# Optimization experiments

Hardware: AMD Instinct MI355X
Metric: run time of the kernel (lower is better)

Reference implementation:

```python
import jax, jax.numpy as jnp
import numpy as np

B, D, CIN, H, W = 2, 6, 3, 96, 96
DIM, NUM_HEADS, DEPTH = 144, 6, 2
WS = (2, 8, 8)   # window size (d, h, w)
SS = (1, 4, 4)   # shift size for odd blocks
HID = int(DIM * 2.0)
TBL = (2 * WS[0] - 1) * (2 * WS[1] - 1) * (2 * WS[2] - 1)  # 675
EPS = 1e-5


def _rpi(ws):
    # pairwise relative position index, same math as WindowAttention.get_position_index
    coords = np.stack(np.meshgrid(np.arange(ws[0]), np.arange(ws[1]), np.arange(ws[2]), indexing='ij'))
    cf = coords.reshape(3, -1).astype(np.int64)
    rc = (cf[:, :, None] - cf[:, None, :]).transpose(1, 2, 0)
    rc[..., 0] += ws[0] - 1
    rc[..., 1] += ws[1] - 1
    rc[..., 2] += ws[2] - 1
    rc[..., 0] *= (2 * ws[1] - 1) * (2 * ws[2] - 1)
    rc[..., 1] *= 2 * ws[2] - 1
    return rc.sum(-1)  # (N, N)


def _win_part_np(x, ws):
    b, d, h, w, c = x.shape
    x = x.reshape(b, d // ws[0], ws[0], h // ws[1], ws[1], w // ws[2], ws[2], c)
    return x.transpose(0, 1, 3, 5, 2, 4, 6, 7).reshape(-1, ws[0] * ws[1] * ws[2], c)


def _attn_mask(Dp, Hp, Wp, ws, ss):
    # static shift-window attention mask, same as compute_mask
    img = np.zeros((1, Dp, Hp, Wp, 1), np.float32)
    cnt = 0
    for d in (slice(-ws[0]), slice(-ws[0], -ss[0]), slice(-ss[0], None)):
        for h in (slice(-ws[1]), slice(-ws[1], -ss[1]), slice(-ss[1], None)):
            for w in (slice(-ws[2]), slice(-ws[2], -ss[2]), slice(-ss[2], None)):
                img[:, d, h, w, :] = cnt
                cnt += 1
    mw = _win_part_np(img, ws)[..., 0]  # (nW, N)
    am = mw[:, None, :] - mw[:, :, None]
    return np.where(am != 0, np.float32(-100.0), np.float32(0.0))


RPI = jnp.asarray(_rpi(WS))            # (N, N) int
MASK = jnp.asarray(_attn_mask(D, H, W, WS, SS))  # (nW, N, N)


def _ln(x, g, b):
    mu = jnp.mean(x, -1, keepdims=True)
    var = jnp.mean(jnp.square(x - mu), -1, keepdims=True)
    return (x - mu) * jax.lax.rsqrt(var + EPS) * g + b


def _win_part(x, ws):
    b, d, h, w, c = x.shape
    x = x.reshape(b, d // ws[0], ws[0], h // ws[1], ws[1], w // ws[2], ws[2], c)
    return x.transpose(0, 1, 3, 5, 2, 4, 6, 7).reshape(-1, ws[0] * ws[1] * ws[2], c)


def _win_rev(xw, ws, b, d, h, w):
    x = xw.reshape(b, d // ws[0], h // ws[1], w // ws[2], ws[0], ws[1], ws[2], -1)
    return x.transpose(0, 1, 4, 2, 5, 3, 6, 7).reshape(b, d, h, w, -1)


def _stl(x, i, shifted, params):
    # one Swin Transformer Layer; x: (B, D, H, W, C)
    n1g, n1b, qkvw, qkvb, rpb, projw, projb, n2g, n2b, fc1w, fc1b, fc2w, fc2b = params
    b, d, h, w, c = x.shape
    hd = c // NUM_HEADS
    scale = hd ** -0.5
    y = _ln(x, n1g[i], n1b[i])
    if shifted:
        y = jnp.roll(y, (-SS[0], -SS[1], -SS[2]), axis=(1, 2, 3))
    xw = _win_part(y, WS)  # (B_, N, C)
    B_, N, _ = xw.shape
    qkv = jnp.einsum('bnc,oc->bno', xw, qkvw[i]) + qkvb[i]
    qkv = qkv.reshape(B_, N, 3, NUM_HEADS, hd).transpose(2, 0, 3, 1, 4)
    q, k, v = qkv[0], qkv[1], qkv[2]
    attn = jnp.einsum('bhnd,bhmd->bhnm', q * scale, k)
    bias = rpb[i][RPI].transpose(2, 0, 1)  # (heads, N, N)
    attn = attn + bias[None]
    if shifted:
        nW = MASK.shape[0]
        attn = attn.reshape(B_ // nW, nW, NUM_HEADS, N, N) + MASK[None, :, None]
        attn = attn.reshape(B_, NUM_HEADS, N, N)
    attn = jax.nn.softmax(attn, axis=-1)
    out = jnp.einsum('bhnm,bhmd->bhnd', attn, v).transpose(0, 2, 1, 3).reshape(B_, N, c)
    out = jnp.einsum('bnc,oc->bno', out, projw[i]) + projb[i]
    y = _win_rev(out, WS, b, d, h, w)
    if shifted:
        y = jnp.roll(y, (SS[0], SS[1], SS[2]), axis=(1, 2, 3))
    x = x + y
    z = _ln(x, n2g[i], n2b[i])
    z = jnp.einsum('bdhwc,oc->bdhwo', z, fc1w[i]) + fc1b[i]
    z = jax.nn.gelu(z, approximate=False)
    z = jnp.einsum('bdhwo,co->bdhwc', z, fc2w[i]) + fc2b[i]
    return x + z


def setup_inputs() -> dict:
    key = jax.random.key(0)
    ks = jax.random.split(key, 8)
    s = 0.02
    return {
        'x': jax.random.normal(ks[0], (B, D, CIN, H, W), jnp.float32),
        'conv_w': jax.random.normal(ks[1], (DIM, CIN, 1, 3, 3), jnp.float32) * s,
        'conv_b': jnp.zeros((DIM,), jnp.float32),
        'ln0_g': jnp.ones((DIM,), jnp.float32),
        'ln0_b': jnp.zeros((DIM,), jnp.float32),
        'n1g': jnp.ones((DEPTH, DIM), jnp.float32),
        'n1b': jnp.zeros((DEPTH, DIM), jnp.float32),
        'qkvw': jax.random.normal(ks[2], (DEPTH, 3 * DIM, DIM), jnp.float32) * s,
        'qkvb': jnp.zeros((DEPTH, 3 * DIM), jnp.float32),
        'rpb': jax.random.normal(ks[3], (DEPTH, TBL, NUM_HEADS), jnp.float32) * s,
        'projw': jax.random.normal(ks[4], (DEPTH, DIM, DIM), jnp.float32) * s,
        'projb': jnp.zeros((DEPTH, DIM), jnp.float32),
        'n2g': jnp.ones((DEPTH, DIM), jnp.float32),
        'n2b': jnp.zeros((DEPTH, DIM), jnp.float32),
        'fc1w': jax.random.normal(ks[5], (DEPTH, HID, DIM), jnp.float32) * s,
        'fc1b': jnp.zeros((DEPTH, HID), jnp.float32),
        'fc2w': jax.random.normal(ks[6], (DEPTH, DIM, HID), jnp.float32) * s,
        'fc2b': jnp.zeros((DEPTH, DIM), jnp.float32),
        'lin_w': jax.random.normal(ks[7], (DIM, DIM), jnp.float32) * s,
        'lin_b': jnp.zeros((DIM,), jnp.float32),
        'ln1_g': jnp.ones((DIM,), jnp.float32),
        'ln1_b': jnp.zeros((DIM,), jnp.float32),
    }


def reference(x, conv_w, conv_b, ln0_g, ln0_b, n1g, n1b, qkvw, qkvb, rpb, projw, projb,
              n2g, n2b, fc1w, fc1b, fc2w, fc2b, lin_w, lin_b, ln1_g, ln1_b):
    # x: (n, d, c, h, w)
    y = x.transpose(0, 2, 1, 3, 4)  # n c d h w
    y = jax.lax.conv_general_dilated(
        y, conv_w, (1, 1, 1), [(0, 0), (1, 1), (1, 1)],
        dimension_numbers=('NCDHW', 'OIDHW', 'NCDHW')) + conv_b[None, :, None, None, None]
    y = y.transpose(0, 2, 3, 4, 1)  # n d h w c
    y = _ln(y, ln0_g, ln0_b)
    y = y.transpose(0, 4, 1, 2, 3)  # n c d h w
    params = (n1g, n1b, qkvw, qkvb, rpb, projw, projb, n2g, n2b, fc1w, fc1b, fc2w, fc2b)
    # RSTB (num_blocks = 1): residual group (STG of DEPTH STLs) + linear + skip
    f = y.transpose(0, 2, 3, 4, 1)  # b d h w c
    for i in range(DEPTH):
        f = _stl(f, i, i % 2 == 1, params)
    f = jnp.einsum('bdhwc,oc->bdhwo', f, lin_w) + lin_b
    y = y + f.transpose(0, 4, 1, 2, 3)
    # trailing LayerNorm and rearrange back to (n, d, c, h, w)
    out = _ln(y.transpose(0, 2, 3, 4, 1), ln1_g, ln1_b)
    return out.transpose(0, 1, 4, 2, 3)
```

## Files before the change

### kernel.cpp

```cpp
#include <hip/hip_runtime.h>
#include <math.h>

#define NTOK 110592
#define NWIN 864
#define TS   15925248

typedef unsigned short u16;
typedef unsigned int   u32;
typedef __attribute__((ext_vector_type(8))) short short8;
typedef __attribute__((ext_vector_type(4))) float float4v;

__device__ __forceinline__ float bf2f(u16 v) { return __uint_as_float(((u32)v) << 16); }
__device__ __forceinline__ u16 f2bf(float f) {
    u32 u = __float_as_uint(f);
    u32 r = u + 0x7fffu + ((u >> 16) & 1u);
    return (u16)(r >> 16);
}
__device__ __forceinline__ void unpack2(u32 u, float& lo, float& hi) {
    lo = __uint_as_float(u << 16);
    hi = __uint_as_float(u & 0xffff0000u);
}
__device__ __forceinline__ u32 pack2(float lo, float hi) {
    return (u32)f2bf(lo) | ((u32)f2bf(hi) << 16);
}
__device__ __forceinline__ float wave_sum(float v) {
    #pragma unroll
    for (int o = 32; o > 0; o >>= 1) v += __shfl_xor(v, o, 64);
    return v;
}

__device__ __forceinline__ void win_to_src(int tw, int shifted, int& sb, int& sd, int& sh, int& sw) {
    int n = tw & 127;
    int win = tw >> 7;
    int ww = win % 12;
    int wh = (win / 12) % 12;
    int rest = win / 144;
    int wd = rest % 3;
    sb = rest / 3;
    int ld = n >> 6, lh = (n >> 3) & 7, lw = n & 7;
    int dr = wd * 2 + ld, hr = wh * 8 + lh, wr = ww * 8 + lw;
    if (shifted) {
        sd = (dr + 1) % 6;
        sh = (hr + 4) % 96;
        sw = (wr + 4) % 96;
    } else {
        sd = dr; sh = hr; sw = wr;
    }
}

__device__ __forceinline__ int tok_region(int t, int wdn, int whn, int wwn) {
    int dr = wdn * 2 + (t >> 6), hr = whn * 8 + ((t >> 3) & 7), wr = wwn * 8 + (t & 7);
    int rd = (dr < 4) ? 0 : ((dr < 5) ? 1 : 2);
    int rh = (hr < 88) ? 0 : ((hr < 92) ? 1 : 2);
    int rw = (wr < 88) ? 0 : ((wr < 92) ? 1 : 2);
    return rd * 9 + rh * 3 + rw;
}

__global__ __launch_bounds__(256) void convert_weights(
    const float* __restrict__ qkvw, const float* __restrict__ projw,
    const float* __restrict__ fc1w, const float* __restrict__ fc2w,
    const float* __restrict__ linw, u16* __restrict__ wbuf,
    const float* __restrict__ rpb, float* __restrict__ bexp)
{
    int i = blockIdx.x * 256 + threadIdx.x;
    if (i < 124416) wbuf[i] = f2bf(qkvw[i]);
    else if (i < 165888) wbuf[i] = f2bf(projw[i - 124416]);
    else if (i < 248832) wbuf[i] = f2bf(fc1w[i - 165888]);
    else if (i < 331776) wbuf[i] = f2bf(fc2w[i - 248832]);
    else if (i < 352512) wbuf[i] = f2bf(linw[i - 331776]);
    else if (i < 549120) {
        int k = i - 352512;
        int n = k & 127, m = (k >> 7) & 127;
        int lh = k >> 14;
        int h = lh % 6, l = lh / 6;
        int rdi = (m >> 6) - (n >> 6) + 1;
        int rhi = ((m >> 3) & 7) - ((n >> 3) & 7) + 7;
        int rwi = (m & 7) - (n & 7) + 7;
        int bi = (rdi * 15 + rhi) * 15 + rwi;
        bexp[k] = rpb[l * 4050 + bi * 6 + h];
    }
}

__global__ __launch_bounds__(256) void conv_ln0_row(
    const float* __restrict__ x, const float* __restrict__ cw, const float* __restrict__ cb,
    const float* __restrict__ g0, const float* __restrict__ b0,
    float* __restrict__ y0)
{
    int bh = blockIdx.x;
    int h = bh % 96, bd = bh / 96;
    int b = bd / 6, d = bd - b * 6;
    __shared__ float ws[192][29];
    __shared__ float xsr[9][100];
    __shared__ float cbias[192], gg[144], bbv[144];
    int tid = threadIdx.x;

    for (int i = tid; i < 9 * 98; i += 256) {
        int row = i / 98, wx = i - row * 98;
        int ci = row / 3, kh = row - 3 * ci;
        int hh = h + kh - 1, wsrc = wx - 1;
        float v = 0.f;
        if (hh >= 0 && hh < 96 && wsrc >= 0 && wsrc < 96)
            v = x[((((size_t)b * 6 + d) * 3 + ci) * 96 + hh) * 96 + wsrc];
        xsr[row][wx] = v;
    }
    for (int i = tid; i < 192 * 27; i += 256) {
        int c = i / 27, j = i - c * 27;
        ws[c][j] = (c < 144) ? cw[c * 27 + j] : 0.f;
    }
    for (int i = tid; i < 192; i += 256) cbias[i] = (i < 144) ? cb[i] : 0.f;
    for (int i = tid; i < 144; i += 256) { gg[i] = g0[i]; bbv[i] = b0[i]; }
    __syncthreads();

    int wv = tid >> 6, lane = tid & 63;
    int p0 = wv * 24;

    float a0[24], a1[24], a2[24];
    #pragma unroll
    for (int k = 0; k < 24; k++) {
        a0[k] = cbias[lane]; a1[k] = cbias[lane + 64]; a2[k] = cbias[lane + 128];
    }

    for (int cikh = 0; cikh < 9; cikh++) {
        const float* xr = &xsr[cikh][p0];
        float xv[26];
        #pragma unroll
        for (int t = 0; t < 26; t++) xv[t] = xr[t];
        #pragma unroll
        for (int kw = 0; kw < 3; kw++) {
            int j = cikh * 3 + kw;
            float w0 = ws[lane][j], w1 = ws[lane + 64][j], w2 = ws[lane + 128][j];
            #pragma unroll
            for (int k = 0; k < 24; k++) {
                float xvv = xv[k + kw];
                a0[k] += w0 * xvv; a1[k] += w1 * xvv; a2[k] += w2 * xvv;
            }
        }
    }

    #pragma unroll
    for (int k = 0; k < 24; k++) {
        int p = p0 + k;
        float v0 = a0[k], v1 = a1[k];
        float v2m = (lane < 16) ? a2[k] : 0.f;
        float s  = wave_sum(v0 + v1 + v2m);
        float s2 = wave_sum(v0 * v0 + v1 * v1 + v2m * v2m);
        float mu = s * (1.f / 144.f);
        float rstd = rsqrtf(fmaxf(s2 * (1.f / 144.f) - mu * mu, 0.f) + 1e-5f);
        size_t o = ((size_t)bh * 96 + p) * 144;
        float r0 = (v0 - mu) * rstd * gg[lane] + bbv[lane];
        float r1 = (v1 - mu) * rstd * gg[lane + 64] + bbv[lane + 64];
        y0[o + lane] = r0;
        y0[o + lane + 64] = r1;
        if (lane < 16) {
            float r2 = (a2[k] - mu) * rstd * gg[lane + 128] + bbv[lane + 128];
            y0[o + lane + 128] = r2;
        }
    }
}

template<int MODE>
__global__ __launch_bounds__(256) void ln_gather(
    const float* __restrict__ in, u16* __restrict__ out,
    const float* __restrict__ g, const float* __restrict__ bt)
{
    int tok = blockIdx.x * 4 + (threadIdx.x >> 6);
    int lane = threadIdx.x & 63;
    int src;
    {
        int b, d, h, w;
        win_to_src(tok, MODE == 2, b, d, h, w);
        src = ((b * 6 + d) * 96 + h) * 96 + w;
    }
    const float2* row = (const float2*)(in + (size_t)src * 144);
    float2 a = row[lane];
    float2 b2 = (lane < 8) ? row[64 + lane] : make_float2(0.f, 0.f);
    float s  = wave_sum(a.x + a.y + b2.x + b2.y);
    float s2 = wave_sum(a.x * a.x + a.y * a.y + b2.x * b2.x + b2.y * b2.y);
    float mu = s * (1.f / 144.f);
    float rstd = rsqrtf(fmaxf(s2 * (1.f / 144.f) - mu * mu, 0.f) + 1e-5f);
    const float2* g2 = (const float2*)g;
    const float2* t2 = (const float2*)bt;
    u32* orow = (u32*)(out + (size_t)tok * 144);
    float2 gg = g2[lane], tt = t2[lane];
    orow[lane] = pack2((a.x - mu) * rstd * gg.x + tt.x, (a.y - mu) * rstd * gg.y + tt.y);
    if (lane < 8) {
        float2 gh = g2[64 + lane], th = t2[64 + lane];
        orow[64 + lane] = pack2((b2.x - mu) * rstd * gh.x + th.x, (b2.y - mu) * rstd * gh.y + th.y);
    }
}

template<int AMODE, int EPI, int SHIFTED, int ADDBIAS, int KTILES>
__global__ __launch_bounds__(192) void mgemm(
    const void* __restrict__ Asrc, const u16* __restrict__ Wt, const float* __restrict__ bias,
    u16* __restrict__ outb, float* __restrict__ fres, const float* __restrict__ y0,
    const float* __restrict__ lng, const float* __restrict__ lnb,
    int a_add, int a_ld, int w_ld, int o_ld, int o_add)
{
    __shared__ u16 As[64 * 152];
    int m0 = blockIdx.y * 64, n0 = blockIdx.x * 144;
    int tid = threadIdx.x;
    int wv3 = tid / 64, lane = tid & 63;
    int mrow = lane & 15, quad = lane >> 4;
    const short8 z8 = {0, 0, 0, 0, 0, 0, 0, 0};

    float4v acc[4][3];
    #pragma unroll
    for (int i = 0; i < 4; i++)
        #pragma unroll
        for (int j = 0; j < 3; j++) acc[i][j] = (float4v){0.f, 0.f, 0.f, 0.f};

    #pragma unroll
    for (int kt = 0; kt < KTILES; kt++) {
        if (kt) __syncthreads();
        if constexpr (AMODE == 5) {
            __shared__ float gs[144], bs[144], ps[64][6];
            for (int i = tid; i < 144; i += 192) { gs[i] = lng[i]; bs[i] = lnb[i]; }
            int r = tid / 3, p = tid - 3 * r;
            int srow = a_add + m0 + r;
            const float4* s4 = (const float4*)((const float*)Asrc + (size_t)srow * 144) + p * 12;
            float4 av[12];
            float s = 0.f, s2 = 0.f;
            #pragma unroll
            for (int q = 0; q < 12; q++) {
                av[q] = s4[q];
                s  += (av[q].x + av[q].y) + (av[q].z + av[q].w);
                s2 += (av[q].x * av[q].x + av[q].y * av[q].y)
                    + (av[q].z * av[q].z + av[q].w * av[q].w);
            }
            ps[r][p] = s; ps[r][3 + p] = s2;
            __syncthreads();
            float S  = ps[r][0] + ps[r][1] + ps[r][2];
            float S2 = ps[r][3] + ps[r][4] + ps[r][5];
            float mu = S * (1.f / 144.f);
            float rstd = rsqrtf(fmaxf(S2 * (1.f / 144.f) - mu * mu, 0.f) + 1e-5f);
            #pragma unroll
            for (int q = 0; q < 12; q++) {
                int n = p * 48 + q * 4;
                *(u32*)&As[r * 152 + n]     = pack2((av[q].x - mu) * rstd * gs[n]     + bs[n],
                                                    (av[q].y - mu) * rstd * gs[n + 1] + bs[n + 1]);
                *(u32*)&As[r * 152 + n + 2] = pack2((av[q].z - mu) * rstd * gs[n + 2] + bs[n + 2],
                                                    (av[q].w - mu) * rstd * gs[n + 3] + bs[n + 3]);
            }
        } else if constexpr (AMODE == 2) {
            const u16* A = (const u16*)Asrc;
            #pragma unroll
            for (int idx = tid; idx < 1152; idx += 192) {
                int r = idx / 18, c4 = idx - r * 18;
                *(short8*)&As[r * 152 + c4 * 8] =
                    *(const short8*)&A[(size_t)(a_add + m0 + r) * a_ld + kt * 144 + c4 * 8];
            }
        } else if constexpr (AMODE == 3) {
            const u16* A = (const u16*)Asrc;
            int chtok = a_ld;
            int cc = m0 / chtok;
            int t0 = m0 - cc * chtok;
            const u16* Ac = A + (size_t)cc * chtok * 144;
            #pragma unroll
            for (int idx = tid; idx < 1152; idx += 192) {
                int r = idx / 18, c4 = idx - r * 18;
                int hh = c4 / 3, sub = c4 - hh * 3;
                *(short8*)&As[r * 152 + c4 * 8] =
                    *(const short8*)&Ac[((size_t)hh * chtok + t0 + r) * 24 + sub * 8];
            }
        } else {
            const float* A = (const float*)Asrc;
            #pragma unroll
            for (int idx = tid; idx < 2304; idx += 192) {
                int r = idx / 36, c4 = idx - r * 36;
                const float4* src4 = (const float4*)&A[(size_t)(a_add + m0 + r) * a_ld + kt * 144];
                float4 v = src4[c4];
                *(u32*)&As[r * 152 + c4 * 4]     = pack2(v.x, v.y);
                *(u32*)&As[r * 152 + c4 * 4 + 2] = pack2(v.z, v.w);
            }
        }
        __syncthreads();

        const u16* Wg = Wt + (size_t)(n0 + wv3 * 48 + mrow) * w_ld + kt * 144;

        #pragma unroll
        for (int ks = 0; ks < 4; ks++) {
            int k0 = ks * 32;
            short8 af[4], bf[3];
            #pragma unroll
            for (int i = 0; i < 4; i++)
                af[i] = *(const short8*)&As[(i * 16 + mrow) * 152 + k0 + quad * 8];
            #pragma unroll
            for (int j = 0; j < 3; j++)
                bf[j] = *(const short8*)&Wg[(size_t)j * 16 * w_ld + k0 + quad * 8];
            #pragma unroll
            for (int i = 0; i < 4; i++)
                #pragma unroll
                for (int j = 0; j < 3; j++)
                    acc[i][j] = __builtin_amdgcn_mfma_f32_16x16x32_bf16(af[i], bf[j], acc[i][j], 0, 0, 0);
        }
        {
            bool tl = (quad < 2);
            short8 af[4], bf[3];
            #pragma unroll
            for (int i = 0; i < 4; i++)
                af[i] = tl ? *(const short8*)&As[(i * 16 + mrow) * 152 + 128 + quad * 8] : z8;
            #pragma unroll
            for (int j = 0; j < 3; j++)
                bf[j] = tl ? *(const short8*)&Wg[(size_t)j * 16 * w_ld + 128 + quad * 8] : z8;
            #pragma unroll
            for (int i = 0; i < 4; i++)
                #pragma unroll
                for (int j = 0; j < 3; j++)
                    acc[i][j] = __builtin_amdgcn_mfma_f32_16x16x32_bf16(af[i], bf[j], acc[i][j], 0, 0, 0);
        }
    }

    if constexpr (EPI == 6) {
        __syncthreads();
        int slot = blockIdx.x;
        #pragma unroll
        for (int i = 0; i < 4; i++)
            #pragma unroll
            for (int reg = 0; reg < 4; reg++) {
                int ml = i * 16 + quad * 4 + reg;
                #pragma unroll
                for (int j = 0; j < 3; j++) {
                    int hn = wv3 * 48 + j * 16 + mrow;
                    float v = acc[i][j][reg];
                    if (ADDBIAS) v += bias[n0 + hn];
                    if (slot == 0) v *= 0.20412414523193154f;
                    As[ml * 152 + hn] = f2bf(v);
                }
            }
        __syncthreads();
        int chtok = o_ld;
        u32* outw = (u32*)outb;
        for (int gi = tid; gi < 4608; gi += 192) {
            int hh = gi / 768;
            int rem = gi - hh * 768;
            int t = rem / 12, dd2 = rem - t * 12;
            outw[(size_t)slot * 72 * chtok + ((size_t)hh * chtok + m0 + t) * 12 + dd2]
                = *(const u32*)&As[t * 152 + hh * 24 + dd2 * 2];
        }
    } else {
        #pragma unroll
        for (int i = 0; i < 4; i++) {
            #pragma unroll
            for (int reg = 0; reg < 4; reg++) {
                int m = m0 + i * 16 + quad * 4 + reg;
                int orow;
                if (EPI == 2 || EPI == 5) {
                    int b, d, h, w;
                    win_to_src(m, SHIFTED, b, d, h, w);
                    orow = ((b * 6 + d) * 96 + h) * 96 + w;
                } else orow = m + o_add;
                #pragma unroll
                for (int j = 0; j < 3; j++) {
                    int n = n0 + wv3 * 48 + j * 16 + mrow;
                    float v = acc[i][j][reg];
                    if (ADDBIAS) v += bias[n];
                    if (EPI == 1) v = 0.5f * v * (1.f + erff(v * 0.70710678118f));
                    if (EPI == 2 || EPI == 3) {
                        fres[(size_t)orow * 144 + n] += v;
                    } else if (EPI == 5) {
                        fres[(size_t)orow * 144 + n] = y0[(size_t)orow * 144 + n] + v;
                    } else {
                        if (EPI == 4) v += y0[(size_t)orow * o_ld + n];
                        outb[(size_t)orow * o_ld + n] = f2bf(v);
                    }
                }
            }
        }
    }
}

template<int SHIFTED>
__global__ __launch_bounds__(256) void attn_mfma(
    const u16* __restrict__ qkv,
    const float* __restrict__ bexp,
    u16* __restrict__ tok_out,
    int win_base, int chtok)
{
    int win = blockIdx.x;
    int head = blockIdx.y;
    __shared__ __align__(16) u16 Pb[4][2048];
    __shared__ __align__(16) u16 Vt[3072];
    __shared__ float invden_s[128];
    __shared__ u32 reg_pack[32];

    int tid = threadIdx.x;
    int wv = tid >> 6, lane = tid & 63;
    int c = lane & 15, quad = lane >> 4;
    int qbase = wv * 32;
    const short8 z8 = {0, 0, 0, 0, 0, 0, 0, 0};
    const float* bh_ = bexp + head * 16384;
    const u16* qb_ = qkv + ((size_t)head * chtok + (size_t)win * 128) * 24;
    const u16* kb_ = qb_ + (size_t)144 * chtok;
    const u16* vb_ = qb_ + (size_t)288 * chtok;
    int cs = (c & 7) << 3;

    int wdn = 0, whn = 0, wwn = 0;
    if (SHIFTED) {
        int wib = (win_base + win) % 432;
        wwn = wib % 12; whn = (wib / 12) % 12; wdn = wib / 144;
    }

    if (tid < 128) {
        const u32* vsrc = (const u32*)(vb_ + (size_t)tid * 24);
        #pragma unroll
        for (int i = 0; i < 12; i++) {
            u32 u = vsrc[i];
            int d0 = 2 * i, d1 = 2 * i + 1;
            Vt[((d0 << 7) + tid) ^ ((d0 & 7) << 3)] = (u16)(u & 0xffffu);
            Vt[((d1 << 7) + tid) ^ ((d1 & 7) << 3)] = (u16)(u >> 16);
        }
    }
    if (SHIFTED && tid < 32) {
        int t0 = tid * 4;
        reg_pack[tid] = (u32)tok_region(t0, wdn, whn, wwn)
                      | ((u32)tok_region(t0 + 1, wdn, whn, wwn) << 8)
                      | ((u32)tok_region(t0 + 2, wdn, whn, wwn) << 16)
                      | ((u32)tok_region(t0 + 3, wdn, whn, wwn) << 24);
    }
    __syncthreads();

    short8 aq[2];
    #pragma unroll
    for (int i = 0; i < 2; i++) {
        aq[i] = z8;
        if (quad < 3)
            aq[i] = *(const short8*)(qb_ + (size_t)(qbase + i * 16 + c) * 24 + quad * 8);
    }

    float4v s_acc[2][8];
    #pragma unroll
    for (int i = 0; i < 2; i++)
        #pragma unroll
        for (int j = 0; j < 8; j++) s_acc[i][j] = (float4v){0.f, 0.f, 0.f, 0.f};

    #pragma unroll
    for (int j = 0; j < 8; j++) {
        short8 kf = z8;
        if (quad < 3)
            kf = *(const short8*)(kb_ + (size_t)(j * 16 + c) * 24 + quad * 8);
        s_acc[0][j] = __builtin_amdgcn_mfma_f32_16x16x32_bf16(kf, aq[0], s_acc[0][j], 0, 0, 0);
        s_acc[1][j] = __builtin_amdgcn_mfma_f32_16x16x32_bf16(kf, aq[1], s_acc[1][j], 0, 0, 0);
    }

    float4v o_acc[2][2];
    #pragma unroll
    for (int i = 0; i < 2; i++)
        #pragma unroll
        for (int jv = 0; jv < 2; jv++) o_acc[i][jv] = (float4v){0.f, 0.f, 0.f, 0.f};

    #pragma unroll
    for (int i = 0; i < 2; i++) {
        int m = qbase + i * 16 + c;
        const float* brow = bh_ + m * 128;
        u32 myreg = SHIFTED ? (u32)tok_region(m, wdn, whn, wwn) : 0u;
        float den = 0.f;
        #pragma unroll
        for (int j = 0; j < 8; j++) {
            float4 bv = *(const float4*)(brow + j * 16 + quad * 4);
            float s0 = s_acc[i][j][0] + bv.x;
            float s1 = s_acc[i][j][1] + bv.y;
            float s2 = s_acc[i][j][2] + bv.z;
            float s3 = s_acc[i][j][3] + bv.w;
            if (SHIFTED) {
                u32 rv = reg_pack[j * 4 + quad];
                s0 += ((rv & 255u) == myreg) ? 0.f : -100.f;
                s1 += (((rv >> 8) & 255u) == myreg) ? 0.f : -100.f;
                s2 += (((rv >> 16) & 255u) == myreg) ? 0.f : -100.f;
                s3 += ((rv >> 24) == myreg) ? 0.f : -100.f;
            }
            float p0 = __expf(s0), p1 = __expf(s1), p2 = __expf(s2), p3 = __expf(s3);
            den += (p0 + p1) + (p2 + p3);
            u32 w0, w1;
            asm("v_cvt_pk_bf16_f32 %0, %1, %2" : "=v"(w0) : "v"(p0), "v"(p1));
            asm("v_cvt_pk_bf16_f32 %0, %1, %2" : "=v"(w1) : "v"(p2), "v"(p3));
            uint2 wpair = make_uint2(w0, w1);
            *(uint2*)&Pb[wv][((c << 7) + j * 16 + quad * 4) ^ cs] = wpair;
        }
        den += __shfl_xor(den, 16, 64);
        den += __shfl_xor(den, 32, 64);
        if (quad == 0) invden_s[m] = 1.f / den;

        #pragma unroll
        for (int ks = 0; ks < 4; ks++) {
            short8 pf  = *(const short8*)&Pb[wv][((c << 7) + ks * 32 + quad * 8) ^ cs];
            short8 vf0 = *(const short8*)&Vt[((c << 7) + ks * 32 + quad * 8) ^ cs];
            short8 vf1 = (c < 8) ? *(const short8*)&Vt[(((16 + c) << 7) + ks * 32 + quad * 8) ^ cs] : z8;
            o_acc[i][0] = __builtin_amdgcn_mfma_f32_16x16x32_bf16(pf, vf0, o_acc[i][0], 0, 0, 0);
            o_acc[i][1] = __builtin_amdgcn_mfma_f32_16x16x32_bf16(pf, vf1, o_acc[i][1], 0, 0, 0);
        }
    }

    float* ob = (float*)&Pb[wv][0];
    #pragma unroll
    for (int i = 0; i < 2; i++)
        #pragma unroll
        for (int jv = 0; jv < 2; jv++) {
            int d = jv * 16 + c;
            if (d < 24) {
                #pragma unroll
                for (int r = 0; r < 4; r++)
                    ob[(i * 16 + quad * 4 + r) * 26 + d] = o_acc[i][jv][r];
            }
        }
    __syncthreads();

    if (tid < 128) {
        const float2* ol = (const float2*)((const float*)&Pb[0][0]
                                           + (tid >> 5) * 1024 + (tid & 31) * 26);
        float inv = invden_s[tid];
        u32* orow = (u32*)tok_out + ((size_t)head * chtok + (size_t)win * 128 + tid) * 12;
        #pragma unroll
        for (int d2 = 0; d2 < 12; d2++) {
            float2 v = ol[d2];
            orow[d2] = pack2(v.x * inv, v.y * inv);
        }
    }
}

__global__ __launch_bounds__(256) void final_ln_out_kernel(
    const u16* __restrict__ gsrc, const float* __restrict__ g, const float* __restrict__ bt,
    float* __restrict__ out)
{
    int bh = blockIdx.x;
    int h = bh % 96, d = (bh / 96) % 6, b = bh / 576;
    __shared__ u16 tile[96][152];
    __shared__ float stat[96][2];
    const u16* src = gsrc + (size_t)bh * 96 * 144;
    for (int i = threadIdx.x; i < 1728; i += 256) {
        int wt = i / 18, c8 = i - wt * 18;
        *(short8*)&tile[wt][c8 * 8] = *(const short8*)&src[wt * 144 + c8 * 8];
    }
    __syncthreads();
    if (threadIdx.x < 96) {
        const u32* row = (const u32*)&tile[threadIdx.x][0];
        float s = 0.f, s2 = 0.f;
        #pragma unroll
        for (int j = 0; j < 72; j++) {
            float lo, hi; unpack2(row[j], lo, hi);
            s += lo + hi; s2 += lo * lo + hi * hi;
        }
        float mu = s * (1.f / 144.f);
        float var = s2 * (1.f / 144.f) - mu * mu;
        stat[threadIdx.x][0] = mu;
        stat[threadIdx.x][1] = rsqrtf(fmaxf(var, 0.f) + 1e-5f);
    }
    __syncthreads();
    size_t obase = ((size_t)(b * 6 + d) * 144) * 9216 + h * 96;
    for (int i = threadIdx.x; i < 96 * 144; i += blockDim.x) {
        int c = i / 96, wt = i - c * 96;
        out[obase + (size_t)c * 9216 + wt] =
            (bf2f(tile[wt][c]) - stat[wt][0]) * stat[wt][1] * g[c] + bt[c];
    }
}

extern "C" void kernel_launch(void* const* d_in, const int* in_sizes, int n_in,
                              void* d_out, int out_size, void* d_ws, size_t ws_size,
                              hipStream_t stream) {
    const float* x     = (const float*)d_in[0];
    const float* convw = (const float*)d_in[1];
    const float* convb = (const float*)d_in[2];
    const float* ln0g  = (const float*)d_in[3];
    const float* ln0b  = (const float*)d_in[4];
    const float* n1g   = (const float*)d_in[5];
    const float* n1b   = (const float*)d_in[6];
    const float* qkvw  = (const float*)d_in[7];
    const float* qkvb  = (const float*)d_in[8];
    const float* rpb   = (const float*)d_in[9];
    const float* projw = (const float*)d_in[10];
    const float* projb = (const float*)d_in[11];
    const float* n2g   = (const float*)d_in[12];
    const float* n2b   = (const float*)d_in[13];
    const float* fc1w  = (const float*)d_in[14];
    const float* fc1b  = (const float*)d_in[15];
    const float* fc2w  = (const float*)d_in[16];
    const float* fc2b  = (const float*)d_in[17];
    const float* linw  = (const float*)d_in[18];
    const float* linb  = (const float*)d_in[19];
    const float* ln1g  = (const float*)d_in[20];
    const float* ln1b  = (const float*)d_in[21];

    char* wp = (char*)d_ws;
    float* f    = (float*)wp;             wp += (size_t)TS * 4;
    u16*   tok  = (u16*)wp;               wp += (size_t)TS * 2;
    u16*   wbuf = (u16*)wp;               wp += 352512ull * 2;
    float* bexp = (float*)wp;             wp += 196608ull * 4;
    u16*   qkvbuf = (u16*)wp;
    size_t rest = ws_size - (size_t)(wp - (char*)d_ws);
    int nch = (rest >= (size_t)NTOK * 432 * 2) ? 1
            : (rest >= (size_t)NTOK * 216 * 2) ? 2 : 4;
    int nm  = (rest >= (size_t)NTOK * 288 * 2) ? 1
            : (rest >= (size_t)NTOK * 144 * 2) ? 2 : 3;
    float* y0 = (float*)d_out;

    convert_weights<<<2145, 256, 0, stream>>>(qkvw, projw, fc1w, fc2w, linw, wbuf, rpb, bexp);
    conv_ln0_row<<<1152, 256, 0, stream>>>(x, convw, convb, ln0g, ln0b, y0);

    for (int layer = 0; layer < 2; ++layer) {
        const u16* qw  = wbuf + (size_t)layer * 62208;
        const u16* pw  = wbuf + 124416 + (size_t)layer * 20736;
        const u16* f1w = wbuf + 165888 + (size_t)layer * 41472;
        const u16* f2w = wbuf + 248832 + (size_t)layer * 41472;
        const float* qb  = qkvb + (size_t)layer * 432;
        const float* pb  = projb + (size_t)layer * 144;
        const float* g1  = n1g + layer * 144;
        const float* b1  = n1b + layer * 144;
        const float* g2  = n2g + layer * 144;
        const float* b2  = n2b + layer * 144;
        const float* f1b = fc1b + (size_t)layer * 288;
        const float* f2b = fc2b + (size_t)layer * 144;
        const float* bx  = bexp + (size_t)layer * 98304;

        if (layer == 0) ln_gather<1><<<NTOK / 4, 256, 0, stream>>>(y0, tok, g1, b1);
        else            ln_gather<2><<<NTOK / 4, 256, 0, stream>>>(f, tok, g1, b1);

        int chtok = NTOK / nch, chwin = NWIN / nch;
        for (int c = 0; c < nch; c++) {
            mgemm<2, 6, 0, 1, 1><<<dim3(3, chtok / 64), 192, 0, stream>>>(
                tok, qw, qb, qkvbuf, nullptr, nullptr, nullptr, nullptr,
                c * chtok, 144, 144, chtok, 0);
            u16* ob = tok + (size_t)c * chtok * 144;
            if (layer == 0)
                attn_mfma<0><<<dim3(chwin, 6), 256, 0, stream>>>(qkvbuf, bx, ob, c * chwin, chtok);
            else
                attn_mfma<1><<<dim3(chwin, 6), 256, 0, stream>>>(qkvbuf, bx, ob, c * chwin, chtok);
        }

        if (layer == 0)
            mgemm<3, 5, 0, 1, 1><<<dim3(1, NTOK / 64), 192, 0, stream>>>(
                tok, pw, pb, nullptr, f, y0, nullptr, nullptr, 0, chtok, 144, 144, 0);
        else
            mgemm<3, 2, 1, 1, 1><<<dim3(1, NTOK / 64), 192, 0, stream>>>(
                tok, pw, pb, nullptr, f, nullptr, nullptr, nullptr, 0, chtok, 144, 144, 0);

        int fcch = NTOK / nm;
        for (int c = 0; c < nm; c++) {
            int mst = c * fcch;
            mgemm<5, 1, 0, 1, 1><<<dim3(2, fcch / 64), 192, 0, stream>>>(
                f, f1w, f1b, qkvbuf, nullptr, nullptr, g2, b2, mst, 144, 144, 288, 0);
            mgemm<2, 3, 0, 1, 2><<<dim3(1, fcch / 64), 192, 0, stream>>>(
                qkvbuf, f2w, f2b, nullptr, f, nullptr, nullptr, nullptr, 0, 288, 288, 144, mst);
        }
    }

    mgemm<0, 4, 0, 1, 1><<<dim3(1, NTOK / 64), 192, 0, stream>>>(
        f, wbuf + 331776, linb, tok, nullptr, y0, nullptr, nullptr, 0, 144, 144, 144, 0);

    final_ln_out_kernel<<<2 * 6 * 96, 256, 0, stream>>>(tok, ln1g, ln1b, (float*)d_out);
}
```

Measured before the change: 789.6 us.

## Fuse LN1 window gather into QKV GEMM and use exp2 softmax

Removes the standalone ln_gather kernel. The QKV GEMM now reads the fp32 activations directly, mapping each row to its (shifted) window source and applying LayerNorm in its prologue, which avoids a full bf16 token round trip through memory. The softmax switches to a raw v_exp_f32 (exp2) by folding log2(e) into the q scale, the relative-position bias table and the mask constant. Bias loads for the second row group are prefetched while the first is processed. The trade-off is that the LN is recomputed in each of the three column blocks of the QKV GEMM, and the gathered reads are less contiguous.

```diff
diff --git a/kernel.cpp b/kernel.cpp
--- a/kernel.cpp
+++ b/kernel.cpp
@@ -27,6 +27,11 @@
     #pragma unroll
     for (int o = 32; o > 0; o >>= 1) v += __shfl_xor(v, o, 64);
     return v;
+}
+__device__ __forceinline__ float fexp2(float x) {
+    float r;
+    asm("v_exp_f32 %0, %1" : "=v"(r) : "v"(x));
+    return r;
 }
 
 __device__ __forceinline__ void win_to_src(int tw, int shifted, int& sb, int& sd, int& sh, int& sw) {
@@ -77,7 +82,7 @@
         int rhi = ((m >> 3) & 7) - ((n >> 3) & 7) + 7;
         int rwi = (m & 7) - (n & 7) + 7;
         int bi = (rdi * 15 + rhi) * 15 + rwi;
-        bexp[k] = rpb[l * 4050 + bi * 6 + h];
+        bexp[k] = rpb[l * 4050 + bi * 6 + h] * 1.4426950408889634f;
     }
 }
 
@@ -158,37 +163,6 @@
     }
 }
 
-template<int MODE>
-__global__ __launch_bounds__(256) void ln_gather(
-    const float* __restrict__ in, u16* __restrict__ out,
-    const float* __restrict__ g, const float* __restrict__ bt)
-{
-    int tok = blockIdx.x * 4 + (threadIdx.x >> 6);
-    int lane = threadIdx.x & 63;
-    int src;
-    {
-        int b, d, h, w;
-        win_to_src(tok, MODE == 2, b, d, h, w);
-        src = ((b * 6 + d) * 96 + h) * 96 + w;
-    }
-    const float2* row = (const float2*)(in + (size_t)src * 144);
-    float2 a = row[lane];
-    float2 b2 = (lane < 8) ? row[64 + lane] : make_float2(0.f, 0.f);
-    float s  = wave_sum(a.x + a.y + b2.x + b2.y);
-    float s2 = wave_sum(a.x * a.x + a.y * a.y + b2.x * b2.x + b2.y * b2.y);
-    float mu = s * (1.f / 144.f);
-    float rstd = rsqrtf(fmaxf(s2 * (1.f / 144.f) - mu * mu, 0.f) + 1e-5f);
-    const float2* g2 = (const float2*)g;
-    const float2* t2 = (const float2*)bt;
-    u32* orow = (u32*)(out + (size_t)tok * 144);
-    float2 gg = g2[lane], tt = t2[lane];
-    orow[lane] = pack2((a.x - mu) * rstd * gg.x + tt.x, (a.y - mu) * rstd * gg.y + tt.y);
-    if (lane < 8) {
-        float2 gh = g2[64 + lane], th = t2[64 + lane];
-        orow[64 + lane] = pack2((b2.x - mu) * rstd * gh.x + th.x, (b2.y - mu) * rstd * gh.y + th.y);
-    }
-}
-
 template<int AMODE, int EPI, int SHIFTED, int ADDBIAS, int KTILES>
 __global__ __launch_bounds__(192) void mgemm(
     const void* __restrict__ Asrc, const u16* __restrict__ Wt, const float* __restrict__ bias,
@@ -212,11 +186,18 @@
     #pragma unroll
     for (int kt = 0; kt < KTILES; kt++) {
         if (kt) __syncthreads();
-        if constexpr (AMODE == 5) {
+        if constexpr (AMODE == 5 || AMODE == 6) {
             __shared__ float gs[144], bs[144], ps[64][6];
             for (int i = tid; i < 144; i += 192) { gs[i] = lng[i]; bs[i] = lnb[i]; }
             int r = tid / 3, p = tid - 3 * r;
-            int srow = a_add + m0 + r;
+            int srow;
+            if constexpr (AMODE == 6) {
+                int bq, dq, hq, wq;
+                win_to_src(a_add + m0 + r, SHIFTED, bq, dq, hq, wq);
+                srow = ((bq * 6 + dq) * 96 + hq) * 96 + wq;
+            } else {
+                srow = a_add + m0 + r;
+            }
             const float4* s4 = (const float4*)((const float*)Asrc + (size_t)srow * 144) + p * 12;
             float4 av[12];
             float s = 0.f, s2 = 0.f;
@@ -323,7 +304,7 @@
                     int hn = wv3 * 48 + j * 16 + mrow;
                     float v = acc[i][j][reg];
                     if (ADDBIAS) v += bias[n0 + hn];
-                    if (slot == 0) v *= 0.20412414523193154f;
+                    if (slot == 0) v *= 0.29448890f;
                     As[ml * 152 + hn] = f2bf(v);
                 }
             }
@@ -427,6 +408,14 @@
             aq[i] = *(const short8*)(qb_ + (size_t)(qbase + i * 16 + c) * 24 + quad * 8);
     }
 
+    float4 bv0[8];
+    {
+        const float* brow = bh_ + (qbase + c) * 128;
+        #pragma unroll
+        for (int j = 0; j < 8; j++)
+            bv0[j] = *(const float4*)(brow + j * 16 + quad * 4);
+    }
+
     float4v s_acc[2][8];
     #pragma unroll
     for (int i = 0; i < 2; i++)
@@ -448,27 +437,26 @@
         #pragma unroll
         for (int jv = 0; jv < 2; jv++) o_acc[i][jv] = (float4v){0.f, 0.f, 0.f, 0.f};
 
-    #pragma unroll
-    for (int i = 0; i < 2; i++) {
-        int m = qbase + i * 16 + c;
-        const float* brow = bh_ + m * 128;
-        u32 myreg = SHIFTED ? (u32)tok_region(m, wdn, whn, wwn) : 0u;
+    u32 myreg0 = SHIFTED ? (u32)tok_region(qbase + c, wdn, whn, wwn) : 0u;
+    u32 myreg1 = SHIFTED ? (u32)tok_region(qbase + 16 + c, wdn, whn, wwn) : 0u;
+    float4 bv1[8];
+
+    {
         float den = 0.f;
         #pragma unroll
         for (int j = 0; j < 8; j++) {
-            float4 bv = *(const float4*)(brow + j * 16 + quad * 4);
-            float s0 = s_acc[i][j][0] + bv.x;
-            float s1 = s_acc[i][j][1] + bv.y;
-            float s2 = s_acc[i][j][2] + bv.z;
-            float s3 = s_acc[i][j][3] + bv.w;
+            float s0 = s_acc[0][j][0] + bv0[j].x;
+            float s1 = s_acc[0][j][1] + bv0[j].y;
+            float s2 = s_acc[0][j][2] + bv0[j].z;
+            float s3 = s_acc[0][j][3] + bv0[j].w;
             if (SHIFTED) {
                 u32 rv = reg_pack[j * 4 + quad];
-                s0 += ((rv & 255u) == myreg) ? 0.f : -100.f;
-                s1 += (((rv >> 8) & 255u) == myreg) ? 0.f : -100.f;
-                s2 += (((rv >> 16) & 255u) == myreg) ? 0.f : -100.f;
-                s3 += ((rv >> 24) == myreg) ? 0.f : -100.f;
-            }
-            float p0 = __expf(s0), p1 = __expf(s1), p2 = __expf(s2), p3 = __expf(s3);
+                s0 += ((rv & 255u) == myreg0) ? 0.f : -144.2695f;
+                s1 += (((rv >> 8) & 255u) == myreg0) ? 0.f : -144.2695f;
+                s2 += (((rv >> 16) & 255u) == myreg0) ? 0.f : -144.2695f;
+                s3 += ((rv >> 24) == myreg0) ? 0.f : -144.2695f;
+            }
+            float p0 = fexp2(s0), p1 = fexp2(s1), p2 = fexp2(s2), p3 = fexp2(s3);
             den += (p0 + p1) + (p2 + p3);
             u32 w0, w1;
             asm("v_cvt_pk_bf16_f32 %0, %1, %2" : "=v"(w0) : "v"(p0), "v"(p1));
@@ -478,15 +466,59 @@
         }
         den += __shfl_xor(den, 16, 64);
         den += __shfl_xor(den, 32, 64);
-        if (quad == 0) invden_s[m] = 1.f / den;
+        if (quad == 0) invden_s[qbase + c] = 1.f / den;
+
+        {
+            const float* brow = bh_ + (qbase + 16 + c) * 128;
+            #pragma unroll
+            for (int j = 0; j < 8; j++)
+                bv1[j] = *(const float4*)(brow + j * 16 + quad * 4);
+        }
 
         #pragma unroll
         for (int ks = 0; ks < 4; ks++) {
             short8 pf  = *(const short8*)&Pb[wv][((c << 7) + ks * 32 + quad * 8) ^ cs];
             short8 vf0 = *(const short8*)&Vt[((c << 7) + ks * 32 + quad * 8) ^ cs];
             short8 vf1 = (c < 8) ? *(const short8*)&Vt[(((16 + c) << 7) + ks * 32 + quad * 8) ^ cs] : z8;
-            o_acc[i][0] = __builtin_amdgcn_mfma_f32_16x16x32_bf16(pf, vf0, o_acc[i][0], 0, 0, 0);
-            o_acc[i][1] = __builtin_amdgcn_mfma_f32_16x16x32_bf16(pf, vf1, o_acc[i][1], 0, 0, 0);
+            o_acc[0][0] = __builtin_amdgcn_mfma_f32_16x16x32_bf16(pf, vf0, o_acc[0][0], 0, 0, 0);
+            o_acc[0][1] = __builtin_amdgcn_mfma_f32_16x16x32_bf16(pf, vf1, o_acc[0][1], 0, 0, 0);
+        }
+    }
+
+    {
+        float den = 0.f;
+        #pragma unroll
+        for (int j = 0; j < 8; j++) {
+            float s0 = s_acc[1][j][0] + bv1[j].x;
+            float s1 = s_acc[1][j][1] + bv1[j].y;
+            float s2 = s_acc[1][j][2] + bv1[j].z;
+            float s3 = s_acc[1][j][3] + bv1[j].w;
+            if (SHIFTED) {
+                u32 rv = reg_pack[j * 4 + quad];
+                s0 += ((rv & 255u) == myreg1) ? 0.f : -144.2695f;
+                s1 += (((rv >> 8) & 255u) == myreg1) ? 0.f : -144.2695f;
+                s2 += (((rv >> 16) & 255u) == myreg1) ? 0.f : -144.2695f;
+                s3 += ((rv >> 24) == myreg1) ? 0.f : -144.2695f;
+            }
+            float p0 = fexp2(s0), p1 = fexp2(s1), p2 = fexp2(s2), p3 = fexp2(s3);
+            den += (p0 + p1) + (p2 + p3);
+            u32 w0, w1;
+            asm("v_cvt_pk_bf16_f32 %0, %1, %2" : "=v"(w0) : "v"(p0), "v"(p1));
+            asm("v_cvt_pk_bf16_f32 %0, %1, %2" : "=v"(w1) : "v"(p2), "v"(p3));
+            uint2 wpair = make_uint2(w0, w1);
+            *(uint2*)&Pb[wv][((c << 7) + j * 16 + quad * 4) ^ cs] = wpair;
+        }
+        den += __shfl_xor(den, 16, 64);
+        den += __shfl_xor(den, 32, 64);
+        if (quad == 0) invden_s[qbase + 16 + c] = 1.f / den;
+
+        #pragma unroll
+        for (int ks = 0; ks < 4; ks++) {
+            short8 pf  = *(const short8*)&Pb[wv][((c << 7) + ks * 32 + quad * 8) ^ cs];
+            short8 vf0 = *(const short8*)&Vt[((c << 7) + ks * 32 + quad * 8) ^ cs];
+            short8 vf1 = (c < 8) ? *(const short8*)&Vt[(((16 + c) << 7) + ks * 32 + quad * 8) ^ cs] : z8;
+            o_acc[1][0] = __builtin_amdgcn_mfma_f32_16x16x32_bf16(pf, vf0, o_acc[1][0], 0, 0, 0);
+            o_acc[1][1] = __builtin_amdgcn_mfma_f32_16x16x32_bf16(pf, vf1, o_acc[1][1], 0, 0, 0);
         }
     }
 
@@ -610,14 +642,17 @@
         const float* f2b = fc2b + (size_t)layer * 144;
         const float* bx  = bexp + (size_t)layer * 98304;
 
-        if (layer == 0) ln_gather<1><<<NTOK / 4, 256, 0, stream>>>(y0, tok, g1, b1);
-        else            ln_gather<2><<<NTOK / 4, 256, 0, stream>>>(f, tok, g1, b1);
-
+        const float* asrc = (layer == 0) ? y0 : f;
         int chtok = NTOK / nch, chwin = NWIN / nch;
         for (int c = 0; c < nch; c++) {
-            mgemm<2, 6, 0, 1, 1><<<dim3(3, chtok / 64), 192, 0, stream>>>(
-                tok, qw, qb, qkvbuf, nullptr, nullptr, nullptr, nullptr,
-                c * chtok, 144, 144, chtok, 0);
+            if (layer == 0)
+                mgemm<6, 6, 0, 1, 1><<<dim3(3, chtok / 64), 192, 0, stream>>>(
+                    asrc, qw, qb, qkvbuf, nullptr, nullptr, g1, b1,
+                    c * chtok, 144, 144, chtok, 0);
+            else
+                mgemm<6, 6, 1, 1, 1><<<dim3(3, chtok / 64), 192, 0, stream>>>(
+                    asrc, qw, qb, qkvbuf, nullptr, nullptr, g1, b1,
+                    c * chtok, 144, 144, chtok, 0);
             u16* ob = tok + (size_t)c * chtok * 144;
             if (layer == 0)
                 attn_mfma<0><<<dim3(chwin, 6), 256, 0, stream>>>(qkvbuf, bx, ob, c * chwin, chtok);
```

New measurement: 754.4 us. 4.5% less time.

## Fuse LayerNorm window gather into QKV GEMM and use exp2 softmax

Applied to the files above, without the earlier changes.

Removes the standalone ln_gather kernel. The QKV GEMM now computes the window-shifted gather and LayerNorm on the fly from the fp32 residual (new AMODE 6), which saves a bf16 token buffer round trip. The softmax is rescaled into base 2: the bias table, the q scale and the mask constant are pre-multiplied by log2(e) so the kernel can call the raw v_exp_f32 instruction. It also raises wave priority around the MFMA blocks in attention. The QKV GEMM now recomputes LayerNorm once for each of its 3 N-tile blocks, which triples that work and the fp32 reads.

```diff
diff --git a/kernel.cpp b/kernel.cpp
--- a/kernel.cpp
+++ b/kernel.cpp
@@ -27,6 +27,11 @@
     #pragma unroll
     for (int o = 32; o > 0; o >>= 1) v += __shfl_xor(v, o, 64);
     return v;
+}
+__device__ __forceinline__ float fexp2(float x) {
+    float r;
+    asm("v_exp_f32 %0, %1" : "=v"(r) : "v"(x));
+    return r;
 }
 
 __device__ __forceinline__ void win_to_src(int tw, int shifted, int& sb, int& sd, int& sh, int& sw) {
@@ -77,7 +82,7 @@
         int rhi = ((m >> 3) & 7) - ((n >> 3) & 7) + 7;
         int rwi = (m & 7) - (n & 7) + 7;
         int bi = (rdi * 15 + rhi) * 15 + rwi;
-        bexp[k] = rpb[l * 4050 + bi * 6 + h];
+        bexp[k] = rpb[l * 4050 + bi * 6 + h] * 1.4426950408889634f;
     }
 }
 
@@ -158,37 +163,6 @@
     }
 }
 
-template<int MODE>
-__global__ __launch_bounds__(256) void ln_gather(
-    const float* __restrict__ in, u16* __restrict__ out,
-    const float* __restrict__ g, const float* __restrict__ bt)
-{
-    int tok = blockIdx.x * 4 + (threadIdx.x >> 6);
-    int lane = threadIdx.x & 63;
-    int src;
-    {
-        int b, d, h, w;
-        win_to_src(tok, MODE == 2, b, d, h, w);
-        src = ((b * 6 + d) * 96 + h) * 96 + w;
-    }
-    const float2* row = (const float2*)(in + (size_t)src * 144);
-    float2 a = row[lane];
-    float2 b2 = (lane < 8) ? row[64 + lane] : make_float2(0.f, 0.f);
-    float s  = wave_sum(a.x + a.y + b2.x + b2.y);
-    float s2 = wave_sum(a.x * a.x + a.y * a.y + b2.x * b2.x + b2.y * b2.y);
-    float mu = s * (1.f / 144.f);
-    float rstd = rsqrtf(fmaxf(s2 * (1.f / 144.f) - mu * mu, 0.f) + 1e-5f);
-    const float2* g2 = (const float2*)g;
-    const float2* t2 = (const float2*)bt;
-    u32* orow = (u32*)(out + (size_t)tok * 144);
-    float2 gg = g2[lane], tt = t2[lane];
-    orow[lane] = pack2((a.x - mu) * rstd * gg.x + tt.x, (a.y - mu) * rstd * gg.y + tt.y);
-    if (lane < 8) {
-        float2 gh = g2[64 + lane], th = t2[64 + lane];
-        orow[64 + lane] = pack2((b2.x - mu) * rstd * gh.x + th.x, (b2.y - mu) * rstd * gh.y + th.y);
-    }
-}
-
 template<int AMODE, int EPI, int SHIFTED, int ADDBIAS, int KTILES>
 __global__ __launch_bounds__(192) void mgemm(
     const void* __restrict__ Asrc, const u16* __restrict__ Wt, const float* __restrict__ bias,
@@ -212,11 +186,18 @@
     #pragma unroll
     for (int kt = 0; kt < KTILES; kt++) {
         if (kt) __syncthreads();
-        if constexpr (AMODE == 5) {
+        if constexpr (AMODE == 5 || AMODE == 6) {
             __shared__ float gs[144], bs[144], ps[64][6];
             for (int i = tid; i < 144; i += 192) { gs[i] = lng[i]; bs[i] = lnb[i]; }
             int r = tid / 3, p = tid - 3 * r;
-            int srow = a_add + m0 + r;
+            int srow;
+            if constexpr (AMODE == 6) {
+                int bq, dq, hq, wq;
+                win_to_src(a_add + m0 + r, SHIFTED, bq, dq, hq, wq);
+                srow = ((bq * 6 + dq) * 96 + hq) * 96 + wq;
+            } else {
+                srow = a_add + m0 + r;
+            }
             const float4* s4 = (const float4*)((const float*)Asrc + (size_t)srow * 144) + p * 12;
             float4 av[12];
             float s = 0.f, s2 = 0.f;
@@ -323,7 +304,7 @@
                     int hn = wv3 * 48 + j * 16 + mrow;
                     float v = acc[i][j][reg];
                     if (ADDBIAS) v += bias[n0 + hn];
-                    if (slot == 0) v *= 0.20412414523193154f;
+                    if (slot == 0) v *= 0.29448890f;
                     As[ml * 152 + hn] = f2bf(v);
                 }
             }
@@ -433,6 +414,7 @@
         #pragma unroll
         for (int j = 0; j < 8; j++) s_acc[i][j] = (float4v){0.f, 0.f, 0.f, 0.f};
 
+    __builtin_amdgcn_s_setprio(1);
     #pragma unroll
     for (int j = 0; j < 8; j++) {
         short8 kf = z8;
@@ -441,6 +423,7 @@
         s_acc[0][j] = __builtin_amdgcn_mfma_f32_16x16x32_bf16(kf, aq[0], s_acc[0][j], 0, 0, 0);
         s_acc[1][j] = __builtin_amdgcn_mfma_f32_16x16x32_bf16(kf, aq[1], s_acc[1][j], 0, 0, 0);
     }
+    __builtin_amdgcn_s_setprio(0);
 
     float4v o_acc[2][2];
     #pragma unroll
@@ -463,12 +446,12 @@
             float s3 = s_acc[i][j][3] + bv.w;
             if (SHIFTED) {
                 u32 rv = reg_pack[j * 4 + quad];
-                s0 += ((rv & 255u) == myreg) ? 0.f : -100.f;
-                s1 += (((rv >> 8) & 255u) == myreg) ? 0.f : -100.f;
-                s2 += (((rv >> 16) & 255u) == myreg) ? 0.f : -100.f;
-                s3 += ((rv >> 24) == myreg) ? 0.f : -100.f;
-            }
-            float p0 = __expf(s0), p1 = __expf(s1), p2 = __expf(s2), p3 = __expf(s3);
+                s0 += ((rv & 255u) == myreg) ? 0.f : -144.2695f;
+                s1 += (((rv >> 8) & 255u) == myreg) ? 0.f : -144.2695f;
+                s2 += (((rv >> 16) & 255u) == myreg) ? 0.f : -144.2695f;
+                s3 += ((rv >> 24) == myreg) ? 0.f : -144.2695f;
+            }
+            float p0 = fexp2(s0), p1 = fexp2(s1), p2 = fexp2(s2), p3 = fexp2(s3);
             den += (p0 + p1) + (p2 + p3);
             u32 w0, w1;
             asm("v_cvt_pk_bf16_f32 %0, %1, %2" : "=v"(w0) : "v"(p0), "v"(p1));
@@ -480,6 +463,7 @@
         den += __shfl_xor(den, 32, 64);
         if (quad == 0) invden_s[m] = 1.f / den;
 
+        __builtin_amdgcn_s_setprio(1);
         #pragma unroll
         for (int ks = 0; ks < 4; ks++) {
             short8 pf  = *(const short8*)&Pb[wv][((c << 7) + ks * 32 + quad * 8) ^ cs];
@@ -488,6 +472,7 @@
             o_acc[i][0] = __builtin_amdgcn_mfma_f32_16x16x32_bf16(pf, vf0, o_acc[i][0], 0, 0, 0);
             o_acc[i][1] = __builtin_amdgcn_mfma_f32_16x16x32_bf16(pf, vf1, o_acc[i][1], 0, 0, 0);
         }
+        __builtin_amdgcn_s_setprio(0);
     }
 
     float* ob = (float*)&Pb[wv][0];
@@ -610,14 +595,17 @@
         const float* f2b = fc2b + (size_t)layer * 144;
         const float* bx  = bexp + (size_t)layer * 98304;
 
-        if (layer == 0) ln_gather<1><<<NTOK / 4, 256, 0, stream>>>(y0, tok, g1, b1);
-        else            ln_gather<2><<<NTOK / 4, 256, 0, stream>>>(f, tok, g1, b1);
-
+        const float* asrc = (layer == 0) ? y0 : f;
         int chtok = NTOK / nch, chwin = NWIN / nch;
         for (int c = 0; c < nch; c++) {
-            mgemm<2, 6, 0, 1, 1><<<dim3(3, chtok / 64), 192, 0, stream>>>(
-                tok, qw, qb, qkvbuf, nullptr, nullptr, nullptr, nullptr,
-                c * chtok, 144, 144, chtok, 0);
+            if (layer == 0)
+                mgemm<6, 6, 0, 1, 1><<<dim3(3, chtok / 64), 192, 0, stream>>>(
+                    asrc, qw, qb, qkvbuf, nullptr, nullptr, g1, b1,
+                    c * chtok, 144, 144, chtok, 0);
+            else
+                mgemm<6, 6, 1, 1, 1><<<dim3(3, chtok / 64), 192, 0, stream>>>(
+                    asrc, qw, qb, qkvbuf, nullptr, nullptr, g1, b1,
+                    c * chtok, 144, 144, chtok, 0);
             u16* ob = tok + (size_t)c * chtok * 144;
             if (layer == 0)
                 attn_mfma<0><<<dim3(chwin, 6), 256, 0, stream>>>(qkvbuf, bx, ob, c * chwin, chtok);
```

New measurement: 764.6 us. 3.2% less time.
